# Kernel tuning notes

Hardware: AMD Instinct MI355X
Metric: run time of the kernel (lower is better)

The kernel has to match this reference:

```python
import jax, jax.numpy as jnp
import numpy as np
from jax import lax

N = 2000        # nodeNum (genes)
D_IN = 256      # encodeDim
D = 256         # decodeDim
K = 10          # topkratio (k nodes kept)
C = K + 2       # cnnChannel
E_GRAPH = 64000
E_TRAIN = 50000
FLAT = C * (127 + 63 + 31)  # 2652, flattened size after conv/pool chain on length-256 signal
BN_INV = 0.9999950000375  # 1/sqrt(1+1e-5), inference BN with running stats (0,1)


def setup_inputs() -> dict:
    key = jax.random.key(0)
    ks = jax.random.split(key, 16)
    s = lambda i, shape: (jax.random.normal(ks[i], shape, jnp.float32) * 0.05)
    inp = {}
    inp["x"] = jax.random.normal(ks[0], (N, D_IN), jnp.float32)
    inp["edge_index"] = jax.random.randint(ks[1], (2, E_GRAPH), 0, N)
    inp["trainEdge"] = jax.random.randint(ks[2], (E_TRAIN, 2), 0, N)
    # SAGEConv: lin_l (neighbor aggregate, with bias) + lin_r (root, no bias)
    inp["Wl"] = s(3, (D, D_IN)); inp["bl"] = jnp.zeros((D,), jnp.float32)
    inp["Wr"] = s(4, (D, D_IN))
    inp["topk_w"] = s(5, (D,))  # TopKPooling attention vector
    inp["c1_w"] = s(6, (C, C, 2)); inp["c1_b"] = jnp.zeros((C,), jnp.float32)
    inp["c2_w"] = s(7, (C, C, 2)); inp["c2_b"] = jnp.zeros((C,), jnp.float32)
    inp["c3_w"] = s(8, (C, C, 2)); inp["c3_b"] = jnp.zeros((C,), jnp.float32)
    for nm in ("bn1", "bn2", "bn3"):
        inp[nm + "_g"] = jnp.ones((C,), jnp.float32)
        inp[nm + "_b"] = jnp.zeros((C,), jnp.float32)
    inp["bn4_g"] = jnp.ones((128,), jnp.float32); inp["bn4_b"] = jnp.zeros((128,), jnp.float32)
    inp["fc1_w"] = s(9, (128, FLAT)); inp["fc1_b"] = jnp.zeros((128,), jnp.float32)
    inp["fc2_w"] = s(10, (1, 128)); inp["fc2_b"] = jnp.zeros((1,), jnp.float32)
    return inp


def _conv1d(x, w, b):
    # x: [B, C, L], w: [O, I, 2]
    y = lax.conv_general_dilated(x, w, (1,), 'VALID', dimension_numbers=('NCH', 'OIH', 'NCH'))
    return y + b[None, :, None]


def _maxpool2(x):
    return lax.reduce_window(x, -jnp.inf, lax.max, (1, 1, 2), (1, 1, 2), 'VALID')


def _bn(x, g, b):
    # eval-mode BatchNorm1d with running_mean=0, running_var=1
    return x * (BN_INV * g)[None, :, None] + b[None, :, None]


def reference(x, edge_index, trainEdge, Wl, bl, Wr, topk_w,
              bn1_g, bn1_b, bn2_g, bn2_b, bn3_g, bn3_b, bn4_g, bn4_b,
              c1_w, c1_b, c2_w, c2_b, c3_w, c3_b, fc1_w, fc1_b, fc2_w, fc2_b):
    src, dst = edge_index[0], edge_index[1]
    # SAGEConv(mean): lin_l(mean_{j in N(i)} x_j) + lin_r(x_i), then ReLU
    agg = jnp.zeros((N, x.shape[1]), x.dtype).at[dst].add(x[src])
    deg = jnp.zeros((N,), x.dtype).at[dst].add(1.0)
    mean = agg / jnp.maximum(deg, 1.0)[:, None]
    h = jax.nn.relu(mean @ Wl.T + bl + x @ Wr.T)  # [N, D]
    # TopKPooling: score = h.w/||w||, keep top K, scale by tanh(score)
    score = h @ topk_w / jnp.linalg.norm(topk_w)
    topv, topi = lax.top_k(score, K)
    topkarr = h[topi] * jnp.tanh(topv)[:, None]  # [K, D]
    # creatDecodeInput, batched: [E, K+2, D]
    a = h[trainEdge[:, 0]][:, None, :]
    b = h[trainEdge[:, 1]][:, None, :]
    c = jnp.broadcast_to(topkarr[None], (trainEdge.shape[0], K, D))
    z = jnp.concatenate([a, b, c], axis=1)
    # calmodel CNN scorer
    z = _maxpool2(jax.nn.relu(_conv1d(_bn(z, bn1_g, bn1_b), c1_w, c1_b))); x1 = z  # [E,C,127]
    z = _maxpool2(jax.nn.relu(_conv1d(_bn(z, bn2_g, bn2_b), c2_w, c2_b))); x2 = z  # [E,C,63]
    z = _maxpool2(jax.nn.relu(_conv1d(_bn(z, bn3_g, bn3_b), c3_w, c3_b))); x3 = z  # [E,C,31]
    z = jnp.concatenate([x1, x2, x3], axis=2).reshape(x1.shape[0], -1)  # [E, FLAT]
    z = z @ fc1_w.T + fc1_b
    z = z * (BN_INV * bn4_g) + bn4_b  # bn4, eval mode
    z = z @ fc2_w.T + fc2_b
    return jax.nn.sigmoid(z).reshape(-1)  # [E]
```

## Files before the change

### kernel.cpp

```cpp
#include <hip/hip_runtime.h>
#include <hip/hip_bf16.h>
#include <math.h>

#define N_NODES 2000
#define DIN 256
#define DD 256
#define KTOP 10
#define CC 12
#define EG 64000
#define ET 50000
#define L1LEN 255
#define P1LEN 127
#define P2LEN 63
#define P3LEN 31
#define FLAT 2652
#define BN_INV 0.9999950000375f
#define CAP 96

typedef float v2 __attribute__((ext_vector_type(2)));

__device__ __forceinline__ v2 v2fma(v2 a, v2 b, v2 c) {
#if __has_builtin(__builtin_elementwise_fma)
    return __builtin_elementwise_fma(a, b, c);
#else
    v2 r; r.x = fmaf(a.x, b.x, c.x); r.y = fmaf(a.y, b.y, c.y); return r;
#endif
}
__device__ __forceinline__ v2 sp(float s) { v2 r; r.x = s; r.y = s; return r; }
__device__ __forceinline__ float fcomp(const float4& q, int c) {
    switch (c & 3) { case 0: return q.x; case 1: return q.y; case 2: return q.z; default: return q.w; }
}

#define OFF_MEAN   0
#define OFF_H      512000
#define OFF_SC     1024000
#define OFF_CNT    1026000
#define OFF_NBR    1028000
#define OFF_TAB    1220000
#define OFF_C1V    (OFF_TAB)
#define OFF_WA     (OFF_TAB + 6144)
#define OFF_WB     (OFF_TAB + 6168)
#define OFF_W2F    (OFF_TAB + 6192)
#define OFF_B2F    (OFF_TAB + 6480)
#define OFF_W3P    (OFF_TAB + 6492)
#define OFF_B3F    (OFF_TAB + 6780)
#define OFF_V2T    (OFF_TAB + 6792)
#define OFF_V3T    (OFF_TAB + 7560)
#define OFF_C0     (OFF_TAB + 7944)

__global__ void k_fill(const int* __restrict__ ei,
                       const float* __restrict__ fc1w, const float* __restrict__ fc1b,
                       const float* __restrict__ fc2w, const float* __restrict__ fc2b,
                       const float* __restrict__ bn4g, const float* __restrict__ bn4b,
                       const float* __restrict__ c1w,
                       const float* __restrict__ c2w, const float* __restrict__ c2b,
                       const float* __restrict__ c3w, const float* __restrict__ c3b,
                       const float* __restrict__ bn1g,
                       const float* __restrict__ bn2g, const float* __restrict__ bn2b,
                       const float* __restrict__ bn3g, const float* __restrict__ bn3b,
                       float* __restrict__ W) {
    const int tid = threadIdx.x, bid = blockIdx.x;
    if (bid < 250) {
        int e = bid * 256 + tid;
        int* cnt = (int*)(W + OFF_CNT);
        int* nbr = (int*)(W + OFF_NBR);
        int dst = ei[EG + e], src = ei[e];
        int slot = atomicAdd(&cnt[dst], 1);
        nbr[dst * CAP + slot] = src;
        return;
    }
    if (bid < 261) {
        int j = (bid - 250) * 256 + tid;
        if (j >= FLAT) return;
        float acc = 0.f;
        for (int k = 0; k < 128; ++k)
            acc += fc1w[k * FLAT + j] * (fc2w[k] * (BN_INV * bn4g[k]));
        int c = j / 221, pos = j - c * 221;
        if (pos < 127)      W[OFF_C1V + (c * 128 + pos) * 4 + 2] = acc;
        else if (pos < 190) W[OFF_V2T + (pos - 127) * 12 + c] = acc;
        else                W[OFF_V3T + (pos - 190) * 12 + c] = acc;
        return;
    }
    for (int t = tid; t < 288; t += 256) {
        int o = t / 24, r = t - o * 24, tt = r / 12, i = r - tt * 12;
        W[OFF_W2F + t] = c2w[o * 24 + i * 2 + tt] * (BN_INV * bn2g[i]);
        W[OFF_W3P + (tt * 12 + i) * 12 + o] = c3w[o * 24 + i * 2 + tt] * (BN_INV * bn3g[i]);
    }
    if (tid < 12) {
        float s2 = c2b[tid], s3 = c3b[tid];
        for (int i = 0; i < 12; ++i) {
            s2 += (c2w[tid * 24 + i * 2] + c2w[tid * 24 + i * 2 + 1]) * bn2b[i];
            s3 += (c3w[tid * 24 + i * 2] + c3w[tid * 24 + i * 2 + 1]) * bn3b[i];
        }
        W[OFF_B2F + tid] = s2;
        W[OFF_B3F + tid] = s3;
    }
    if (tid < 24) {
        int tt = tid / 12, o = tid - tt * 12;
        W[OFF_WA + tid] = c1w[o * 24 + tt] * (BN_INV * bn1g[0]);
        W[OFF_WB + tid] = c1w[o * 24 + 2 + tt] * (BN_INV * bn1g[1]);
    }
    if (tid == 0) {
        float c = fc2b[0];
        for (int k = 0; k < 128; ++k)
            c += fc2w[k] * (fc1b[k] * (BN_INV * bn4g[k]) + bn4b[k]);
        W[OFF_C0] = c;
    }
}

__global__ void k_gather(const float* __restrict__ x, float* __restrict__ W) {
    int w = threadIdx.x >> 6, lane = threadIdx.x & 63;
    int n = blockIdx.x * 4 + w;
    const int* cnt = (const int*)(W + OFF_CNT);
    const int* nbr = (const int*)(W + OFF_NBR);
    int dg = cnt[n];
    const int* row = nbr + n * CAP;
    float4 acc = make_float4(0.f, 0.f, 0.f, 0.f);
    int j = 0;
    for (; j + 4 <= dg; j += 4) {
        int s0 = row[j], s1 = row[j + 1], s2 = row[j + 2], s3 = row[j + 3];
        float4 v0 = *(const float4*)(x + s0 * DIN + lane * 4);
        float4 v1 = *(const float4*)(x + s1 * DIN + lane * 4);
        float4 v2_ = *(const float4*)(x + s2 * DIN + lane * 4);
        float4 v3 = *(const float4*)(x + s3 * DIN + lane * 4);
        acc.x += v0.x + v1.x + v2_.x + v3.x;
        acc.y += v0.y + v1.y + v2_.y + v3.y;
        acc.z += v0.z + v1.z + v2_.z + v3.z;
        acc.w += v0.w + v1.w + v2_.w + v3.w;
    }
    for (; j < dg; ++j) {
        int s0 = row[j];
        float4 v0 = *(const float4*)(x + s0 * DIN + lane * 4);
        acc.x += v0.x; acc.y += v0.y; acc.z += v0.z; acc.w += v0.w;
    }
    float rd = 1.0f / fmaxf((float)dg, 1.0f);
    *(float4*)(W + OFF_MEAN + n * DIN + lane * 4) =
        make_float4(acc.x * rd, acc.y * rd, acc.z * rd, acc.w * rd);
}

__global__ void k_sage(const float* __restrict__ x, const float* __restrict__ Wl,
                       const float* __restrict__ bl, const float* __restrict__ Wr,
                       const float* __restrict__ tw, float* __restrict__ W) {
    __shared__ float As[32][33], Xs[32][33], Bls[32][33], Brs[32][33];
    const float* mean = W + OFF_MEAN;
    float* h = W + OFF_H;
    float* sc = W + OFF_SC;
    int tid = threadIdx.x;
    int tx = tid & 15, ty = tid >> 4;
    int n0 = blockIdx.y * 32, d0 = blockIdx.x * 32;
    int lrow = tid >> 3, lcol = (tid & 7) * 4;
    v2 acc0 = sp(0.f), acc1 = sp(0.f);
    for (int k0 = 0; k0 < DIN; k0 += 32) {
        int gn = n0 + lrow;
        float4 av, xv;
        if (gn < N_NODES) {
            av = *(const float4*)(mean + gn * DIN + k0 + lcol);
            xv = *(const float4*)(x + gn * DIN + k0 + lcol);
        } else {
            av = make_float4(0.f, 0.f, 0.f, 0.f); xv = av;
        }
        As[lrow][lcol + 0] = av.x; As[lrow][lcol + 1] = av.y;
        As[lrow][lcol + 2] = av.z; As[lrow][lcol + 3] = av.w;
        Xs[lrow][lcol + 0] = xv.x; Xs[lrow][lcol + 1] = xv.y;
        Xs[lrow][lcol + 2] = xv.z; Xs[lrow][lcol + 3] = xv.w;
        int gd = d0 + lrow;
        float4 bv = *(const float4*)(Wl + gd * DIN + k0 + lcol);
        float4 rv = *(const float4*)(Wr + gd * DIN + k0 + lcol);
        Bls[lrow][lcol + 0] = bv.x; Bls[lrow][lcol + 1] = bv.y;
        Bls[lrow][lcol + 2] = bv.z; Bls[lrow][lcol + 3] = bv.w;
        Brs[lrow][lcol + 0] = rv.x; Brs[lrow][lcol + 1] = rv.y;
        Brs[lrow][lcol + 2] = rv.z; Brs[lrow][lcol + 3] = rv.w;
        __syncthreads();
#pragma unroll
        for (int kk = 0; kk < 32; ++kk) {
            v2 b; b.x = Bls[2 * tx][kk]; b.y = Bls[2 * tx + 1][kk];
            v2 r; r.x = Brs[2 * tx][kk]; r.y = Brs[2 * tx + 1][kk];
            acc0 = v2fma(b, sp(As[2 * ty][kk]), acc0);
            acc0 = v2fma(r, sp(Xs[2 * ty][kk]), acc0);
            acc1 = v2fma(b, sp(As[2 * ty + 1][kk]), acc1);
            acc1 = v2fma(r, sp(Xs[2 * ty + 1][kk]), acc1);
        }
        __syncthreads();
    }
    float tw0 = tw[d0 + 2 * tx], tw1 = tw[d0 + 2 * tx + 1];
    float bl0 = bl[d0 + 2 * tx], bl1 = bl[d0 + 2 * tx + 1];
    float hv[2][2];
    hv[0][0] = fmaxf(acc0.x + bl0, 0.f); hv[0][1] = fmaxf(acc0.y + bl1, 0.f);
    hv[1][0] = fmaxf(acc1.x + bl0, 0.f); hv[1][1] = fmaxf(acc1.y + bl1, 0.f);
    float s0 = fmaf(hv[0][0], tw0, hv[0][1] * tw1);
    float s1 = fmaf(hv[1][0], tw0, hv[1][1] * tw1);
#pragma unroll
    for (int i = 0; i < 2; ++i) {
        int n = n0 + 2 * ty + i;
        if (n < N_NODES) {
            h[n * DD + d0 + 2 * tx] = hv[i][0];
            h[n * DD + d0 + 2 * tx + 1] = hv[i][1];
        }
    }
#pragma unroll
    for (int off = 8; off > 0; off >>= 1) {
        s0 += __shfl_xor(s0, off, 64);
        s1 += __shfl_xor(s1, off, 64);
    }
    if (tx == 0) {
        int n = n0 + 2 * ty;
        if (n < N_NODES) atomicAdd(&sc[n], s0);
        if (n + 1 < N_NODES) atomicAdd(&sc[n + 1], s1);
    }
}

__global__ void k_topk(const float* __restrict__ tw, const float* __restrict__ c1w,
                       const float* __restrict__ c1b, const float* __restrict__ bn1g,
                       const float* __restrict__ bn1b, float* __restrict__ W) {
    __shared__ float s_tt[KTOP];
    __shared__ int   s_ti[KTOP];
    int tid = threadIdx.x;
    if (tid < 64) {
        int lane = tid;
        const float* sc = W + OFF_SC;
        float v[32];
#pragma unroll
        for (int s = 0; s < 32; ++s) {
            int idx = s * 64 + lane;
            v[s] = (idx < N_NODES) ? sc[idx] : -1e30f;
        }
        float p = 0.f;
#pragma unroll
        for (int k = 0; k < 4; ++k) { float t = tw[lane + 64 * k]; p = fmaf(t, t, p); }
#pragma unroll
        for (int off = 32; off > 0; off >>= 1) p += __shfl_xor(p, off, 64);
        float rnorm = 1.0f / sqrtf(p);
#pragma unroll
        for (int k = 0; k < KTOP; ++k) {
            float m = v[0];
#pragma unroll
            for (int s = 1; s < 32; ++s) m = fmaxf(m, v[s]);
#pragma unroll
            for (int off = 32; off > 0; off >>= 1) m = fmaxf(m, __shfl_xor(m, off, 64));
            int cand = 0x7fffffff;
#pragma unroll
            for (int s = 0; s < 32; ++s)
                if (v[s] == m) cand = min(cand, s * 64 + lane);
#pragma unroll
            for (int off = 32; off > 0; off >>= 1) cand = min(cand, __shfl_xor(cand, off, 64));
#pragma unroll
            for (int s = 0; s < 32; ++s)
                if (s * 64 + lane == cand) v[s] = -1e30f;
            if (lane == 0) { s_ti[k] = cand; s_tt[k] = tanhf(m * rnorm); }
        }
    }
    __syncthreads();
    const float* h = W + OFF_H;
    for (int jj = tid; jj < CC * L1LEN; jj += 256) {
        int o = jj / L1LEN, l = jj - o * L1LEN;
        float sum = c1b[o];
        sum += (c1w[o * 24 + 0] + c1w[o * 24 + 1]) * bn1b[0];
        sum += (c1w[o * 24 + 2] + c1w[o * 24 + 3]) * bn1b[1];
#pragma unroll
        for (int r = 0; r < KTOP; ++r) {
            int ch = r + 2;
            float tv = s_tt[r];
            float sr = BN_INV * bn1g[ch];
            float br = bn1b[ch];
            const float* hr = h + s_ti[r] * DD;
            float v0 = fmaf(hr[l], tv * sr, br);
            float v1 = fmaf(hr[l + 1], tv * sr, br);
            sum += c1w[o * 24 + ch * 2] * v0 + c1w[o * 24 + ch * 2 + 1] * v1;
        }
        W[OFF_C1V + (o * 128 + (l >> 1)) * 4 + (l & 1)] = sum;
    }
}

__launch_bounds__(256, 6)
__global__ void k_edges(const float* __restrict__ h, const int* __restrict__ te,
                        const float* __restrict__ W, float* __restrict__ out) {
    __shared__ float s1[4][CC][128];
    const int tid = threadIdx.x;
    const int w = tid >> 6, lane = tid & 63;
    const int e = blockIdx.x * 4 + w;

    int na = __builtin_amdgcn_readfirstlane(te[2 * e]);
    int nb = __builtin_amdgcn_readfirstlane(te[2 * e + 1]);
    const float* ha = h + na * DD;
    const float* hb = h + nb * DD;
    const float4* c1v = (const float4*)(W + OFF_C1V);
    const float* wa = W + OFF_WA;
    const float* wb = W + OFF_WB;
    const float* w2 = W + OFF_W2F;
    const float* b2 = W + OFF_B2F;
    const float* w3p = W + OFF_W3P;
    const float* b3 = W + OFF_B3F;
    const float4* v2t = (const float4*)(W + OFF_V2T);
    const float4* v3t = (const float4*)(W + OFF_V3T);

    float dot0 = 0.f, dot1 = 0.f;

#pragma unroll
    for (int rep = 0; rep < 2; ++rep) {
        int p = lane + rep * 64;
        if (p < P1LEN) {
            float2 a01 = *(const float2*)(ha + 2 * p);
            float  a2  = ha[2 * p + 2];
            float2 b01 = *(const float2*)(hb + 2 * p);
            float  b2v = hb[2 * p + 2];
            v2 va0; va0.x = a01.x; va0.y = a01.y;
            v2 va1; va1.x = a01.y; va1.y = a2;
            v2 vb0; vb0.x = b01.x; vb0.y = b01.y;
            v2 vb1; vb1.x = b01.y; vb1.y = b2v;
#pragma unroll
            for (int o = 0; o < CC; ++o) {
                float4 cv = c1v[o * 128 + p];
                v2 u; u.x = cv.x; u.y = cv.y;
                u = v2fma(sp(wa[o]), va0, u);
                u = v2fma(sp(wa[12 + o]), va1, u);
                u = v2fma(sp(wb[o]), vb0, u);
                u = v2fma(sp(wb[12 + o]), vb1, u);
                float r = fmaxf(fmaxf(u.x, u.y), 0.0f);
                s1[w][o][p] = r;
                if (o & 1) dot1 = fmaf(r, cv.z, dot1);
                else       dot0 = fmaf(r, cv.z, dot0);
            }
        }
    }
    __builtin_amdgcn_wave_barrier();

    float r2[CC];
#pragma unroll
    for (int i = 0; i < CC; ++i) r2[i] = 0.f;
    if (lane < P2LEN) {
        int p = lane;
        float4 q0 = v2t[p * 3 + 0], q1 = v2t[p * 3 + 1], q2 = v2t[p * 3 + 2];
        v2 evo[CC], ovE[CC];
#pragma unroll
        for (int i = 0; i < CC; ++i) {
            float2 t2 = *(const float2*)(&s1[w][i][2 * p]);
            float e1 = s1[w][i][2 * p + 2];
            evo[i].x = t2.x; evo[i].y = t2.y;
            ovE[i].x = t2.y; ovE[i].y = e1;
        }
#pragma unroll
        for (int o = 0; o < CC; ++o) {
            v2 a = sp(b2[o]);
#pragma unroll
            for (int i = 0; i < CC; ++i) {
                a = v2fma(sp(w2[o * 24 + i]), evo[i], a);
                a = v2fma(sp(w2[o * 24 + 12 + i]), ovE[i], a);
            }
            float r = fmaxf(fmaxf(a.x, a.y), 0.0f);
            r2[o] = r;
            float vv = (o < 4) ? fcomp(q0, o) : (o < 8) ? fcomp(q1, o) : fcomp(q2, o);
            if (o & 1) dot1 = fmaf(r, vv, dot1);
            else       dot0 = fmaf(r, vv, dot0);
        }
    }

    {
        float vq1[CC];
#pragma unroll
        for (int i = 0; i < CC; ++i) vq1[i] = __shfl_down(r2[i], 1, 64);
        bool take = ((lane & 1) == 0) && (lane < 62);
        int t = lane >> 1;
        float4 u0 = v3t[t * 3 + 0], u1 = v3t[t * 3 + 1], u2 = v3t[t * 3 + 2];
#pragma unroll
        for (int op = 0; op < 6; ++op) {
            int o = 2 * op;
            v2 a; a.x = b3[o]; a.y = b3[o + 1];
#pragma unroll
            for (int i = 0; i < CC; ++i) {
                a = v2fma(sp(r2[i]), *(const v2*)(w3p + i * 12 + o), a);
                a = v2fma(sp(vq1[i]), *(const v2*)(w3p + (12 + i) * 12 + o), a);
            }
            float pnx = __shfl_xor(a.x, 1, 64);
            float pny = __shfl_xor(a.y, 1, 64);
            float r0 = fmaxf(fmaxf(a.x, pnx), 0.0f);
            float r1 = fmaxf(fmaxf(a.y, pny), 0.0f);
            if (take) {
                float w0 = (o < 4) ? fcomp(u0, o) : (o < 8) ? fcomp(u1, o) : fcomp(u2, o);
                float w1 = (o + 1 < 4) ? fcomp(u0, o + 1) : (o + 1 < 8) ? fcomp(u1, o + 1) : fcomp(u2, o + 1);
                dot0 = fmaf(r0, w0, dot0);
                dot1 = fmaf(r1, w1, dot1);
            }
        }
    }

    float dot = dot0 + dot1;
#pragma unroll
    for (int off = 32; off > 0; off >>= 1) dot += __shfl_xor(dot, off, 64);
    if (lane == 0) {
        float tt = dot + W[OFF_C0];
        out[e] = 1.0f / (1.0f + expf(-tt));
    }
}

extern "C" void kernel_launch(void* const* d_in, const int* in_sizes, int n_in,
                              void* d_out, int out_size, void* d_ws, size_t ws_size,
                              hipStream_t stream) {
    const float* x    = (const float*)d_in[0];
    const int*   ei   = (const int*)d_in[1];
    const int*   te   = (const int*)d_in[2];
    const float* Wl   = (const float*)d_in[3];
    const float* bl   = (const float*)d_in[4];
    const float* Wr   = (const float*)d_in[5];
    const float* tw   = (const float*)d_in[6];
    const float* c1w  = (const float*)d_in[7];
    const float* c1b  = (const float*)d_in[8];
    const float* c2w  = (const float*)d_in[9];
    const float* c2b  = (const float*)d_in[10];
    const float* c3w  = (const float*)d_in[11];
    const float* c3b  = (const float*)d_in[12];
    const float* bn1g = (const float*)d_in[13];
    const float* bn1b = (const float*)d_in[14];
    const float* bn2g = (const float*)d_in[15];
    const float* bn2b = (const float*)d_in[16];
    const float* bn3g = (const float*)d_in[17];
    const float* bn3b = (const float*)d_in[18];
    const float* bn4g = (const float*)d_in[19];
    const float* bn4b = (const float*)d_in[20];
    const float* fc1w = (const float*)d_in[21];
    const float* fc1b = (const float*)d_in[22];
    const float* fc2w = (const float*)d_in[23];
    const float* fc2b = (const float*)d_in[24];
    float* W   = (float*)d_ws;
    float* out = (float*)d_out;

    hipMemsetAsync(W + OFF_SC, 0, 4000 * sizeof(float), stream);
    k_fill<<<262, 256, 0, stream>>>(ei, fc1w, fc1b, fc2w, fc2b, bn4g, bn4b, c1w,
                                    c2w, c2b, c3w, c3b, bn1g, bn2g, bn2b, bn3g, bn3b, W);
    k_gather<<<500, 256, 0, stream>>>(x, W);
    dim3 g2(8, 63);
    k_sage<<<g2, 256, 0, stream>>>(x, Wl, bl, Wr, tw, W);
    k_topk<<<1, 256, 0, stream>>>(tw, c1w, c1b, bn1g, bn1b, W);
    k_edges<<<ET / 4, 256, 0, stream>>>(W + OFF_H, te, W, out);
}
```

Baseline: 164.6 us.

## Split gather per node across two waves, parallelize topk conv, shrink edge blocks

```diff
diff --git a/kernel.cpp b/kernel.cpp
--- a/kernel.cpp
+++ b/kernel.cpp
@@ -27,9 +27,6 @@
 #endif
 }
 __device__ __forceinline__ v2 sp(float s) { v2 r; r.x = s; r.y = s; return r; }
-__device__ __forceinline__ float fcomp(const float4& q, int c) {
-    switch (c & 3) { case 0: return q.x; case 1: return q.y; case 2: return q.z; default: return q.w; }
-}
 
 #define OFF_MEAN   0
 #define OFF_H      512000
@@ -110,32 +107,31 @@
 
 __global__ void k_gather(const float* __restrict__ x, float* __restrict__ W) {
     int w = threadIdx.x >> 6, lane = threadIdx.x & 63;
-    int n = blockIdx.x * 4 + w;
+    int n = blockIdx.x * 2 + (w >> 1);
+    int fo = (w & 1) * 128 + lane * 2;
     const int* cnt = (const int*)(W + OFF_CNT);
     const int* nbr = (const int*)(W + OFF_NBR);
     int dg = cnt[n];
     const int* row = nbr + n * CAP;
-    float4 acc = make_float4(0.f, 0.f, 0.f, 0.f);
+    float ax = 0.f, ay = 0.f;
     int j = 0;
     for (; j + 4 <= dg; j += 4) {
         int s0 = row[j], s1 = row[j + 1], s2 = row[j + 2], s3 = row[j + 3];
-        float4 v0 = *(const float4*)(x + s0 * DIN + lane * 4);
-        float4 v1 = *(const float4*)(x + s1 * DIN + lane * 4);
-        float4 v2_ = *(const float4*)(x + s2 * DIN + lane * 4);
-        float4 v3 = *(const float4*)(x + s3 * DIN + lane * 4);
-        acc.x += v0.x + v1.x + v2_.x + v3.x;
-        acc.y += v0.y + v1.y + v2_.y + v3.y;
-        acc.z += v0.z + v1.z + v2_.z + v3.z;
-        acc.w += v0.w + v1.w + v2_.w + v3.w;
+        float2 v0 = *(const float2*)(x + s0 * DIN + fo);
+        float2 v1 = *(const float2*)(x + s1 * DIN + fo);
+        float2 v2_ = *(const float2*)(x + s2 * DIN + fo);
+        float2 v3 = *(const float2*)(x + s3 * DIN + fo);
+        ax += v0.x + v1.x + v2_.x + v3.x;
+        ay += v0.y + v1.y + v2_.y + v3.y;
     }
     for (; j < dg; ++j) {
         int s0 = row[j];
-        float4 v0 = *(const float4*)(x + s0 * DIN + lane * 4);
-        acc.x += v0.x; acc.y += v0.y; acc.z += v0.z; acc.w += v0.w;
+        float2 v0 = *(const float2*)(x + s0 * DIN + fo);
+        ax += v0.x; ay += v0.y;
     }
     float rd = 1.0f / fmaxf((float)dg, 1.0f);
-    *(float4*)(W + OFF_MEAN + n * DIN + lane * 4) =
-        make_float4(acc.x * rd, acc.y * rd, acc.z * rd, acc.w * rd);
+    float2 o2; o2.x = ax * rd; o2.y = ay * rd;
+    *(float2*)(W + OFF_MEAN + n * DIN + fo) = o2;
 }
 
 __global__ void k_sage(const float* __restrict__ x, const float* __restrict__ Wl,
@@ -251,8 +247,8 @@
     }
     __syncthreads();
     const float* h = W + OFF_H;
-    for (int jj = tid; jj < CC * L1LEN; jj += 256) {
-        int o = jj / L1LEN, l = jj - o * L1LEN;
+    const int o = blockIdx.x;
+    for (int l = tid; l < L1LEN; l += 256) {
         float sum = c1b[o];
         sum += (c1w[o * 24 + 0] + c1w[o * 24 + 1]) * bn1b[0];
         sum += (c1w[o * 24 + 2] + c1w[o * 24 + 3]) * bn1b[1];
@@ -271,13 +267,13 @@
     }
 }
 
-__launch_bounds__(256, 6)
+__launch_bounds__(128, 6)
 __global__ void k_edges(const float* __restrict__ h, const int* __restrict__ te,
                         const float* __restrict__ W, float* __restrict__ out) {
-    __shared__ float s1[4][CC][128];
+    __shared__ float s1[2][CC][128];
     const int tid = threadIdx.x;
     const int w = tid >> 6, lane = tid & 63;
-    const int e = blockIdx.x * 4 + w;
+    const int e = blockIdx.x * 2 + w;
 
     int na = __builtin_amdgcn_readfirstlane(te[2 * e]);
     int nb = __builtin_amdgcn_readfirstlane(te[2 * e + 1]);
@@ -329,7 +325,6 @@
     for (int i = 0; i < CC; ++i) r2[i] = 0.f;
     if (lane < P2LEN) {
         int p = lane;
-        float4 q0 = v2t[p * 3 + 0], q1 = v2t[p * 3 + 1], q2 = v2t[p * 3 + 2];
         v2 evo[CC], ovE[CC];
 #pragma unroll
         for (int i = 0; i < CC; ++i) {
@@ -338,19 +333,25 @@
             evo[i].x = t2.x; evo[i].y = t2.y;
             ovE[i].x = t2.y; ovE[i].y = e1;
         }
-#pragma unroll
-        for (int o = 0; o < CC; ++o) {
-            v2 a = sp(b2[o]);
-#pragma unroll
-            for (int i = 0; i < CC; ++i) {
-                a = v2fma(sp(w2[o * 24 + i]), evo[i], a);
-                a = v2fma(sp(w2[o * 24 + 12 + i]), ovE[i], a);
+        const float4* vrow = v2t + p * 3;
+#pragma unroll
+        for (int g = 0; g < 3; ++g) {
+            float4 q = vrow[g];
+#pragma unroll
+            for (int oo = 0; oo < 4; ++oo) {
+                const int o = g * 4 + oo;
+                v2 a = sp(b2[o]);
+#pragma unroll
+                for (int i = 0; i < CC; ++i) {
+                    a = v2fma(sp(w2[o * 24 + i]), evo[i], a);
+                    a = v2fma(sp(w2[o * 24 + 12 + i]), ovE[i], a);
+                }
+                float r = fmaxf(fmaxf(a.x, a.y), 0.0f);
+                r2[o] = r;
+                float vv = (oo == 0) ? q.x : (oo == 1) ? q.y : (oo == 2) ? q.z : q.w;
+                if (o & 1) dot1 = fmaf(r, vv, dot1);
+                else       dot0 = fmaf(r, vv, dot0);
             }
-            float r = fmaxf(fmaxf(a.x, a.y), 0.0f);
-            r2[o] = r;
-            float vv = (o < 4) ? fcomp(q0, o) : (o < 8) ? fcomp(q1, o) : fcomp(q2, o);
-            if (o & 1) dot1 = fmaf(r, vv, dot1);
-            else       dot0 = fmaf(r, vv, dot0);
         }
     }
 
@@ -360,10 +361,10 @@
         for (int i = 0; i < CC; ++i) vq1[i] = __shfl_down(r2[i], 1, 64);
         bool take = ((lane & 1) == 0) && (lane < 62);
         int t = lane >> 1;
-        float4 u0 = v3t[t * 3 + 0], u1 = v3t[t * 3 + 1], u2 = v3t[t * 3 + 2];
+        float4 ug0 = v3t[t * 3 + 0], ug1 = v3t[t * 3 + 1], ug2 = v3t[t * 3 + 2];
 #pragma unroll
         for (int op = 0; op < 6; ++op) {
-            int o = 2 * op;
+            const int o = 2 * op;
             v2 a; a.x = b3[o]; a.y = b3[o + 1];
 #pragma unroll
             for (int i = 0; i < CC; ++i) {
@@ -375,8 +376,9 @@
             float r0 = fmaxf(fmaxf(a.x, pnx), 0.0f);
             float r1 = fmaxf(fmaxf(a.y, pny), 0.0f);
             if (take) {
-                float w0 = (o < 4) ? fcomp(u0, o) : (o < 8) ? fcomp(u1, o) : fcomp(u2, o);
-                float w1 = (o + 1 < 4) ? fcomp(u0, o + 1) : (o + 1 < 8) ? fcomp(u1, o + 1) : fcomp(u2, o + 1);
+                const float4 ug = (op < 2) ? ug0 : (op < 4) ? ug1 : ug2;
+                float w0 = (op & 1) ? ug.z : ug.x;
+                float w1 = (op & 1) ? ug.w : ug.y;
                 dot0 = fmaf(r0, w0, dot0);
                 dot1 = fmaf(r1, w1, dot1);
             }
@@ -426,9 +428,9 @@
     hipMemsetAsync(W + OFF_SC, 0, 4000 * sizeof(float), stream);
     k_fill<<<262, 256, 0, stream>>>(ei, fc1w, fc1b, fc2w, fc2b, bn4g, bn4b, c1w,
                                     c2w, c2b, c3w, c3b, bn1g, bn2g, bn2b, bn3g, bn3b, W);
-    k_gather<<<500, 256, 0, stream>>>(x, W);
+    k_gather<<<1000, 256, 0, stream>>>(x, W);
     dim3 g2(8, 63);
     k_sage<<<g2, 256, 0, stream>>>(x, Wl, bl, Wr, tw, W);
-    k_topk<<<1, 256, 0, stream>>>(tw, c1w, c1b, bn1g, bn1b, W);
-    k_edges<<<ET / 4, 256, 0, stream>>>(W + OFF_H, te, W, out);
-}
+    k_topk<<<12, 256, 0, stream>>>(tw, c1w, c1b, bn1g, bn1b, W);
+    k_edges<<<ET / 2, 128, 0, stream>>>(W + OFF_H, te, W, out);
+}
```

Result: no change. 161.7 us (-1.8%).
